# Performance work log

Hardware: AMD Instinct MI355X
Metric: run time of the kernel (lower is better)

## Reference

```python
import jax, jax.numpy as jnp
import numpy as np

NEG_SLOPE = 0.2  # LeakyReLU slope in GAT attention
HEADS = 10

def gat_layer(x, src, dst, W, a_src, a_dst, b, H, C, N):
    # x: [N, F_in]; W: [F_in, H*C]; a_src/a_dst: [H, C]; b: [C]
    h = (x @ W).reshape(N, H, C)                      # [N, H, C]
    e_s = (h * a_src).sum(-1)                         # [N, H]
    e_d = (h * a_dst).sum(-1)                         # [N, H]
    e = jax.nn.leaky_relu(e_s[src] + e_d[dst], NEG_SLOPE)  # [E, H]
    m = jax.ops.segment_max(e, dst, num_segments=N)
    m = jnp.where(jnp.isfinite(m), m, 0.0)
    p = jnp.exp(e - m[dst])                           # [E, H]
    denom = jax.ops.segment_sum(p, dst, num_segments=N)
    alpha = p / (denom[dst] + 1e-16)                  # [E, H]
    out = jax.ops.segment_sum(alpha[:, :, None] * h[src], dst, num_segments=N)  # [N, H, C]
    return out.mean(1) + b                            # heads averaged (concat=False)


def setup_inputs() -> dict:
    key = jax.random.key(0)
    N, E, F, CLS = 10000, 160000, 24, 24
    ks = jax.random.split(key, 24)
    p = lambda k, shp: 0.1 * jax.random.normal(k, shp, dtype=jnp.float32)
    return {
        "x": jax.random.normal(ks[0], (N, F), dtype=jnp.float32),
        "edge_index": jax.random.randint(ks[1], (2, E), 0, N, dtype=jnp.int64),
        "batch": jnp.sort(jax.random.randint(ks[2], (N,), 0, 64, dtype=jnp.int64)),
        "W0": p(ks[3], (F, 16)), "b0": p(ks[4], (16,)),
        "Wc1": p(ks[5], (16, HEADS * 32)), "as1": p(ks[6], (HEADS, 32)), "ad1": p(ks[7], (HEADS, 32)), "bc1": p(ks[8], (32,)),
        "Wc2": p(ks[9], (32, HEADS * 64)), "as2": p(ks[10], (HEADS, 64)), "ad2": p(ks[11], (HEADS, 64)), "bc2": p(ks[12], (64,)),
        "Wc3": p(ks[13], (64, HEADS * 128)), "as3": p(ks[14], (HEADS, 128)), "ad3": p(ks[15], (HEADS, 128)), "bc3": p(ks[16], (128,)),
        "W1": p(ks[17], (128, 256)), "b1": p(ks[18], (256,)),
        "W2": p(ks[19], (256, CLS)), "b2": p(ks[20], (CLS,)),
    }


def reference(x, edge_index, batch, W0, b0, Wc1, as1, ad1, bc1, Wc2, as2, ad2, bc2,
              Wc3, as3, ad3, bc3, W1, b1, W2, b2):
    N = x.shape[0]
    self_loop = jnp.arange(N, dtype=edge_index.dtype)
    src = jnp.concatenate([edge_index[0], self_loop])
    dst = jnp.concatenate([edge_index[1], self_loop])
    h = jax.nn.elu(x @ W0 + b0)
    h = jax.nn.elu(gat_layer(h, src, dst, Wc1, as1, ad1, bc1, HEADS, 32, N))
    h = jax.nn.elu(gat_layer(h, src, dst, Wc2, as2, ad2, bc2, HEADS, 64, N))
    h = jax.nn.elu(gat_layer(h, src, dst, Wc3, as3, ad3, bc3, HEADS, 128, N))
    h = jax.nn.elu(h @ W1 + b1)
    # dropout is identity in eval mode
    logits = h @ W2 + b2
    return jax.nn.log_softmax(logits, axis=1)
```

## Files before the change

kernel.cpp:

```cpp
#include <hip/hip_runtime.h>
#include <hip/hip_bf16.h>
#include <math.h>

#define NHEADS 10

typedef unsigned short ushort_t;
typedef unsigned int uint_t;

typedef __attribute__((ext_vector_type(4))) float f32x4;
typedef __attribute__((ext_vector_type(8))) short short8;

__device__ __forceinline__ float bu2f(ushort_t u){ return __uint_as_float(((uint_t)u)<<16); }
__device__ __forceinline__ ushort_t f2bu(float f){
    uint_t b = __float_as_uint(f);
    return (ushort_t)((b + 0x7FFFu + ((b>>16)&1u)) >> 16);
}

__global__ void k_count(const int* eidx, int E, int N, int* cnt){
    int e = blockIdx.x*blockDim.x + threadIdx.x;
    int ET = E + N;
    if(e >= ET) return;
    int d = (e < E) ? eidx[E + e] : (e - E);
    atomicAdd(&cnt[d], 1);
}

__global__ void k_scan(int* cnt, int N, int ET, int* indptr){
    __shared__ int lds[1024];
    int t = threadIdx.x;
    int chunk = (N + 1023)/1024;
    int base = t*chunk;
    int s = 0;
    for(int i=0;i<chunk;i++){ int idx=base+i; if(idx<N) s += cnt[idx]; }
    lds[t]=s;
    __syncthreads();
    for(int off=1; off<1024; off<<=1){
        int v = (t>=off)? lds[t-off] : 0;
        __syncthreads();
        lds[t]+=v;
        __syncthreads();
    }
    int run = lds[t]-s;
    for(int i=0;i<chunk;i++){
        int idx=base+i;
        if(idx<N){
            int c = cnt[idx];
            indptr[idx]=run;
            cnt[idx]=run;
            run += c;
        }
    }
    if(t==0) indptr[N]=ET;
}

__global__ void k_fill(const int* eidx, int E, int N, int* cursor, int* srcs){
    int e = blockIdx.x*blockDim.x + threadIdx.x;
    int ET = E + N;
    if(e >= ET) return;
    int s, d;
    if(e < E){ s = eidx[e]; d = eidx[E+e]; } else { s = e-E; d = e-E; }
    int pos = atomicAdd(&cursor[d], 1);
    srcs[pos] = s;
}

__global__ void k_sortw(const int* indptr, int* srcs, int N){
    int wid  = (blockIdx.x*blockDim.x + threadIdx.x) >> 6;
    int lane = threadIdx.x & 63;
    if(wid >= N) return;
    int p0 = indptr[wid], p1 = indptr[wid+1];
    int deg = p1 - p0;
    if(deg <= 1) return;
    if(deg <= 64){
        int v = (lane < deg) ? srcs[p0+lane] : 0x7FFFFFFF;
        #pragma unroll
        for(int k=2; k<=64; k<<=1){
            #pragma unroll
            for(int j=k>>1; j>0; j>>=1){
                int partner = __shfl_xor(v, j, 64);
                bool dir   = ((lane & k) == 0);
                bool small = ((lane & j) == 0);
                int mn = min(v, partner), mx = max(v, partner);
                v = (dir == small) ? mn : mx;
            }
        }
        if(lane < deg) srcs[p0+lane] = v;
    } else if(lane == 0){
        for(int i=p0+1;i<p1;i++){
            int v2 = srcs[i]; int j=i-1;
            while(j>=p0 && srcs[j]>v2){ srcs[j+1]=srcs[j]; j--; }
            srcs[j+1]=v2;
        }
    }
}

__global__ void k_trans(const float* __restrict__ W, ushort_t* __restrict__ WT,
                        int K, int KP, int HC){
    int idx = blockIdx.x*blockDim.x + threadIdx.x;
    if(idx >= HC*KP) return;
    int c = idx / KP, k = idx % KP;
    WT[idx] = (k < K) ? f2bu(W[(size_t)k*HC + c]) : (ushort_t)0;
}

__global__ void k_fc0(const float* x, const float* W0, const float* b0, float* out, int N){
    int idx = blockIdx.x*blockDim.x+threadIdx.x;
    if(idx >= N*16) return;
    int n = idx>>4, c = idx&15;
    float acc = b0[c];
    #pragma unroll
    for(int k=0;k<24;k++) acc += x[n*24+k] * W0[k*16+c];
    out[idx] = acc>0.f ? acc : expm1f(acc);
}

template<int K, int KP, int EPI, int OUTBF16>
__global__ void __launch_bounds__(256, 4)
k_gemm(const float* __restrict__ A, const ushort_t* __restrict__ BT,
       const float* __restrict__ bias, void* __restrict__ Cmat,
       int N, int HC){
    int t = threadIdx.x;
    int w = t >> 6, lane = t & 63;
    int lr = lane & 15, lk = lane >> 4;
    int row0 = blockIdx.x*64, col0 = blockIdx.y*64;
    int row = row0 + w*16 + lr;

    f32x4 acc[4];
    #pragma unroll
    for(int f=0; f<4; f++) acc[f] = (f32x4){0.f,0.f,0.f,0.f};

    #pragma unroll
    for(int kb = 0; kb < K; kb += 32){
        int k0 = kb + lk*8;
        short8 af = {0,0,0,0,0,0,0,0};
        if(row < N && k0 < K){
            const float* ap = &A[(size_t)row*K + k0];
            float4 a0 = *(const float4*)ap;
            float4 a1 = *(const float4*)(ap + 4);
            af[0]=(short)f2bu(a0.x); af[1]=(short)f2bu(a0.y);
            af[2]=(short)f2bu(a0.z); af[3]=(short)f2bu(a0.w);
            af[4]=(short)f2bu(a1.x); af[5]=(short)f2bu(a1.y);
            af[6]=(short)f2bu(a1.z); af[7]=(short)f2bu(a1.w);
        }
        #pragma unroll
        for(int f=0; f<4; f++){
            int col = col0 + f*16 + lr;
            short8 bf = *(const short8*)&BT[(size_t)col*KP + k0];
            acc[f] = __builtin_amdgcn_mfma_f32_16x16x32_bf16(af, bf, acc[f], 0, 0, 0);
        }
    }

    #pragma unroll
    for(int f=0; f<4; f++){
        #pragma unroll
        for(int j=0; j<4; j++){
            int r = row0 + w*16 + lk*4 + j;
            if(r >= N) continue;
            int col = col0 + f*16 + lr;
            float v = acc[f][j];
            if(EPI){
                v += bias[col];
                v = v>0.f ? v : expm1f(v);
            }
            if(OUTBF16) ((ushort_t*)Cmat)[(size_t)r*HC + col] = f2bu(v);
            else        ((float*)Cmat)[(size_t)r*HC + col] = v;
        }
    }
}

template<int C>
__global__ void k_attn(const ushort_t* hf, const float* a_s, const float* a_d,
                       float* es, float* ed, int N){
    int tid = blockIdx.x*blockDim.x + threadIdx.x;
    if(tid >= N*NHEADS*4) return;
    int q   = tid & 3;
    int idx = tid >> 2;
    int n = idx/NHEADS, h = idx%NHEADS;
    constexpr int CQ = C/4;
    const ushort_t* hp = hf + (size_t)n*NHEADS*C + h*C + q*CQ;
    const float* asp = a_s + h*C + q*CQ;
    const float* adp = a_d + h*C + q*CQ;
    float s=0.f, d=0.f;
    #pragma unroll
    for(int cb=0; cb<CQ/8; cb++){
        uint4 qv = *(const uint4*)(hp + cb*8);
        uint_t uu[4] = {qv.x, qv.y, qv.z, qv.w};
        #pragma unroll
        for(int j=0;j<4;j++){
            float f0 = __uint_as_float(uu[j]<<16);
            float f1 = __uint_as_float(uu[j] & 0xFFFF0000u);
            int c = cb*8 + j*2;
            s += f0*asp[c] + f1*asp[c+1];
            d += f0*adp[c] + f1*adp[c+1];
        }
    }
    s += __shfl_xor(s, 1, 64); s += __shfl_xor(s, 2, 64);
    d += __shfl_xor(d, 1, 64); d += __shfl_xor(d, 2, 64);
    if(q == 0){ es[idx]=s; ed[idx]=d; }
}

template<int C>
__global__ void __launch_bounds__(256, 4)
k_fused(const int* __restrict__ indptr, const int* __restrict__ srcs,
        const float* __restrict__ es, const float* __restrict__ ed,
        const ushort_t* __restrict__ hf, const float* __restrict__ bc,
        float* __restrict__ out, int N)
{
    __shared__ float wlds[4][64*NHEADS];
    __shared__ float stat[4][NHEADS];
    __shared__ int   degs[4];
    int wslot = threadIdx.x >> 6;
    int lane  = threadIdx.x & 63;
    int n = (blockIdx.x << 2) + wslot;
    bool valid = (n < N);
    int p0 = 0, deg = 0;
    if(valid){ p0 = indptr[n]; deg = indptr[n+1] - p0; }
    if(lane == 0) degs[wslot] = deg;
    __syncthreads();
    int maxdeg = max(max(degs[0],degs[1]), max(degs[2],degs[3]));
    int nch = (maxdeg + 63) >> 6;
    float* wl = wlds[wslot];

    int e6 = lane/10, h6 = lane%10;
    float edv = (valid && lane < 60) ? ed[n*NHEADS + h6] : 0.f;

    float den = 0.f;
    for(int c = 0; c < nch; c++){
        int base = c << 6;
        int lim = deg - base; if(lim > 64) lim = 64;
        if(valid && lane < 60){
            for(int i = e6; i < lim; i += 6){
                float v = es[(size_t)srcs[p0+base+i]*NHEADS + h6] + edv;
                v = (v >= 0.f) ? v : 0.2f*v;
                wl[i*NHEADS + h6] = expf(fminf(v, 60.f));
            }
        }
        __syncthreads();
        if(valid && lane < NHEADS){
            for(int i = 0; i < lim; i++) den += wl[i*NHEADS + lane];
        }
        if(nch > 1) __syncthreads();
    }
    if(valid && lane < NHEADS) stat[wslot][lane] = 1.f/(den + 1e-30f);
    __syncthreads();

    constexpr int TPN = C/8;
    constexpr int EG  = 64/TPN;
    int local = lane % TPN, eg = lane / TPN;
    int c8 = local*8;
    float dinv_r[NHEADS];
    #pragma unroll
    for(int h=0; h<NHEADS; h++) dinv_r[h] = stat[wslot][h];
    float acc[8];
    #pragma unroll
    for(int i=0;i<8;i++) acc[i]=0.f;

    for(int c = 0; c < nch; c++){
        int base = c << 6;
        int lim = deg - base; if(lim > 64) lim = 64;
        if(nch > 1){
            if(valid && lane < 60){
                for(int i = e6; i < lim; i += 6){
                    float v = es[(size_t)srcs[p0+base+i]*NHEADS + h6] + edv;
                    v = (v >= 0.f) ? v : 0.2f*v;
                    wl[i*NHEADS + h6] = expf(fminf(v, 60.f));
                }
            }
            __syncthreads();
        }
        if(valid){
            for(int i = eg; i < lim; i += EG){
                int s = srcs[p0+base+i];
                const ushort_t* hp = hf + (size_t)s*NHEADS*C + c8;
                const float* wp = &wl[i*NHEADS];
                #pragma unroll
                for(int h=0;h<NHEADS;h++){
                    uint4 q = *(const uint4*)(hp + h*C);
                    float wd = wp[h]*dinv_r[h];
                    acc[0] += wd * __uint_as_float(q.x<<16);
                    acc[1] += wd * __uint_as_float(q.x & 0xFFFF0000u);
                    acc[2] += wd * __uint_as_float(q.y<<16);
                    acc[3] += wd * __uint_as_float(q.y & 0xFFFF0000u);
                    acc[4] += wd * __uint_as_float(q.z<<16);
                    acc[5] += wd * __uint_as_float(q.z & 0xFFFF0000u);
                    acc[6] += wd * __uint_as_float(q.w<<16);
                    acc[7] += wd * __uint_as_float(q.w & 0xFFFF0000u);
                }
            }
        }
        if(nch > 1) __syncthreads();
    }

    #pragma unroll
    for(int s = TPN; s < 64; s <<= 1){
        #pragma unroll
        for(int i=0;i<8;i++) acc[i] += __shfl_xor(acc[i], s, 64);
    }
    if(valid && eg == 0){
        float4 v0, v1;
        #pragma unroll
        for(int i=0;i<8;i++){
            float v = acc[i]*(1.f/NHEADS) + bc[c8+i];
            v = v>0.f ? v : expm1f(v);
            if(i<4) ((float*)&v0)[i] = v; else ((float*)&v1)[i-4] = v;
        }
        *(float4*)&out[(size_t)n*C + c8]     = v0;
        *(float4*)&out[(size_t)n*C + c8 + 4] = v1;
    }
}

__global__ void k_head(const float* hin, const float* W2, const float* b2v, float* out, int N){
    int grp  = threadIdx.x/32;
    int lane = threadIdx.x%32;
    int n = blockIdx.x*8 + grp;
    if(n>=N) return;
    float acc = -1e30f;
    if(lane < 24){
        acc = b2v[lane];
        for(int k=0;k<256;k++) acc += hin[n*256+k]*W2[k*24+lane];
    }
    float mx = acc;
    for(int off=16; off; off>>=1) mx = fmaxf(mx, __shfl_xor(mx, off, 32));
    float ex = (lane<24)? expf(acc-mx) : 0.f;
    float sm = ex;
    for(int off=16; off; off>>=1) sm += __shfl_xor(sm, off, 32);
    if(lane<24) out[n*24+lane] = acc - mx - logf(sm);
}

extern "C" void kernel_launch(void* const* d_in, const int* in_sizes, int n_in,
                              void* d_out, int out_size, void* d_ws, size_t ws_size,
                              hipStream_t stream) {
    const float* x   = (const float*)d_in[0];
    const int*  eidx = (const int*)d_in[1];
    const float* W0 = (const float*)d_in[3];  const float* b0 = (const float*)d_in[4];
    const float* Wc1= (const float*)d_in[5];  const float* as1= (const float*)d_in[6];
    const float* ad1= (const float*)d_in[7];  const float* bc1= (const float*)d_in[8];
    const float* Wc2= (const float*)d_in[9];  const float* as2= (const float*)d_in[10];
    const float* ad2= (const float*)d_in[11]; const float* bc2= (const float*)d_in[12];
    const float* Wc3= (const float*)d_in[13]; const float* as3= (const float*)d_in[14];
    const float* ad3= (const float*)d_in[15]; const float* bc3= (const float*)d_in[16];
    const float* W1 = (const float*)d_in[17]; const float* b1 = (const float*)d_in[18];
    const float* W2 = (const float*)d_in[19]; const float* b2 = (const float*)d_in[20];
    float* out = (float*)d_out;

    const int N  = in_sizes[0]/24;
    const int E  = in_sizes[1]/2;
    const int ET = E + N;

    char* w = (char*)d_ws;
    size_t off = 0;
    auto alloc = [&](size_t bytes)->void* {
        void* p = w + off;
        off = (off + bytes + 255) & ~(size_t)255;
        return p;
    };
    int*   cnt    = (int*)  alloc((size_t)N*4);
    int*   indptr = (int*)  alloc((size_t)(N+1)*4);
    int*   srcs   = (int*)  alloc((size_t)ET*4);
    float* es     = (float*)alloc((size_t)N*NHEADS*4);
    float* ed     = (float*)alloc((size_t)N*NHEADS*4);
    float* nfA    = (float*)alloc((size_t)N*256*4);
    float* nfB    = (float*)alloc((size_t)N*256*4);
    ushort_t* hf  = (ushort_t*)alloc((size_t)N*1280*2);
    ushort_t* WT1 = (ushort_t*)alloc((size_t)320*32*2);
    ushort_t* WT2 = (ushort_t*)alloc((size_t)640*32*2);
    ushort_t* WT3 = (ushort_t*)alloc((size_t)1280*64*2);
    ushort_t* WT4 = (ushort_t*)alloc((size_t)256*128*2);

    k_trans<<<(320*32+255)/256,256,0,stream>>>(Wc1, WT1, 16, 32, 320);
    k_trans<<<(640*32+255)/256,256,0,stream>>>(Wc2, WT2, 32, 32, 640);
    k_trans<<<(1280*64+255)/256,256,0,stream>>>(Wc3, WT3, 64, 64, 1280);
    k_trans<<<(256*128+255)/256,256,0,stream>>>(W1, WT4, 128, 128, 256);

    hipMemsetAsync(cnt, 0, (size_t)N*4, stream);
    int gE = (ET+255)/256;
    k_count<<<gE,256,0,stream>>>(eidx, E, N, cnt);
    k_scan <<<1,1024,0,stream>>>(cnt, N, ET, indptr);
    k_fill <<<gE,256,0,stream>>>(eidx, E, N, cnt, srcs);
    k_sortw<<<((size_t)N*64+255)/256,256,0,stream>>>(indptr, srcs, N);

    int gA   = (N*NHEADS*4+255)/256;
    int gRow = (N+63)/64;
    int gNode = (N+3)/4;

    k_fc0<<<(N*16+255)/256,256,0,stream>>>(x, W0, b0, nfA, N);

    k_gemm<16,32,0,1><<<dim3(gRow,320/64),256,0,stream>>>(nfA, WT1, nullptr, hf, N, 320);
    k_attn<32><<<gA,256,0,stream>>>(hf, as1, ad1, es, ed, N);
    k_fused<32><<<gNode,256,0,stream>>>(indptr, srcs, es, ed, hf, bc1, nfB, N);

    k_gemm<32,32,0,1><<<dim3(gRow,640/64),256,0,stream>>>(nfB, WT2, nullptr, hf, N, 640);
    k_attn<64><<<gA,256,0,stream>>>(hf, as2, ad2, es, ed, N);
    k_fused<64><<<gNode,256,0,stream>>>(indptr, srcs, es, ed, hf, bc2, nfA, N);

    k_gemm<64,64,0,1><<<dim3(gRow,1280/64),256,0,stream>>>(nfA, WT3, nullptr, hf, N, 1280);
    k_attn<128><<<gA,256,0,stream>>>(hf, as3, ad3, es, ed, N);
    k_fused<128><<<gNode,256,0,stream>>>(indptr, srcs, es, ed, hf, bc3, nfB, N);

    k_gemm<128,128,1,0><<<dim3(gRow,256/64),256,0,stream>>>(nfB, WT4, b1, nfA, N, 256);
    k_head<<<(N+7)/8,256,0,stream>>>(nfA, W2, b2, out, N);
}
```

Baseline: 298.2 us.

## Phase neighbor gathers by source-index window and merge weight transpose launches

Splits the sorted source neighbors of each node into P index windows and walks them phase by phase, with a block barrier between phases. The waves of a block then gather feature rows from the same region of the bf16 feature array at roughly the same time, which should improve L2 locality. The four weight-transpose launches are also merged into one kernel to save launch overhead. The cost is up to P extra __syncthreads per block, and the multi-chunk path now folds the inverse denominator into the stored weights for chunks after the first.

```diff
diff --git a/kernel.cpp b/kernel.cpp
--- a/kernel.cpp
+++ b/kernel.cpp
@@ -92,12 +92,17 @@
     }
 }
 
-__global__ void k_trans(const float* __restrict__ W, ushort_t* __restrict__ WT,
-                        int K, int KP, int HC){
+__global__ void k_trans_all(const float* __restrict__ W1c,const float* __restrict__ W2c,
+                            const float* __restrict__ W3c,const float* __restrict__ W4c,
+                            ushort_t* T1,ushort_t* T2,ushort_t* T3,ushort_t* T4){
     int idx = blockIdx.x*blockDim.x + threadIdx.x;
-    if(idx >= HC*KP) return;
-    int c = idx / KP, k = idx % KP;
-    WT[idx] = (k < K) ? f2bu(W[(size_t)k*HC + c]) : (ushort_t)0;
+    if(idx < 10240){ int c=idx/32, k=idx%32; T1[idx] = (k<16)? f2bu(W1c[(size_t)k*320+c]) : (ushort_t)0; return; }
+    idx -= 10240;
+    if(idx < 20480){ int c=idx/32, k=idx%32; T2[idx] = f2bu(W2c[(size_t)k*640+c]); return; }
+    idx -= 20480;
+    if(idx < 81920){ int c=idx/64, k=idx%64; T3[idx] = f2bu(W3c[(size_t)k*1280+c]); return; }
+    idx -= 81920;
+    if(idx < 32768){ int c=idx/128, k=idx%128; T4[idx] = f2bu(W4c[(size_t)k*256+c]); return; }
 }
 
 __global__ void k_fc0(const float* x, const float* W0, const float* b0, float* out, int N){
@@ -195,7 +200,7 @@
     if(q == 0){ es[idx]=s; ed[idx]=d; }
 }
 
-template<int C>
+template<int C, int P>
 __global__ void __launch_bounds__(256, 4)
 k_fused(const int* __restrict__ indptr, const int* __restrict__ srcs,
         const float* __restrict__ es, const float* __restrict__ ed,
@@ -251,22 +256,14 @@
     #pragma unroll
     for(int i=0;i<8;i++) acc[i]=0.f;
 
-    for(int c = 0; c < nch; c++){
-        int base = c << 6;
-        int lim = deg - base; if(lim > 64) lim = 64;
-        if(nch > 1){
-            if(valid && lane < 60){
-                for(int i = e6; i < lim; i += 6){
-                    float v = es[(size_t)srcs[p0+base+i]*NHEADS + h6] + edv;
-                    v = (v >= 0.f) ? v : 0.2f*v;
-                    wl[i*NHEADS + h6] = expf(fminf(v, 60.f));
-                }
-            }
-            __syncthreads();
-        }
-        if(valid){
-            for(int i = eg; i < lim; i += EG){
-                int s = srcs[p0+base+i];
+    if(nch == 1){
+        int lim = deg;
+        int win = (N + P - 1)/P;
+        int i = eg;
+        for(int ph = 0; ph < P; ph++){
+            int bound = win*(ph+1);
+            while(i < lim && srcs[p0+i] < bound){
+                int s = srcs[p0+i];
                 const ushort_t* hp = hf + (size_t)s*NHEADS*C + c8;
                 const float* wp = &wl[i*NHEADS];
                 #pragma unroll
@@ -282,9 +279,48 @@
                     acc[6] += wd * __uint_as_float(q.w<<16);
                     acc[7] += wd * __uint_as_float(q.w & 0xFFFF0000u);
                 }
-            }
-        }
-        if(nch > 1) __syncthreads();
+                i += EG;
+            }
+            __syncthreads();
+        }
+    } else {
+        for(int c = 0; c < nch; c++){
+            int base = c << 6;
+            int lim = deg - base; if(lim > 64) lim = 64;
+            if(c > 0){
+                if(valid && lane < 60){
+                    for(int i = e6; i < lim; i += 6){
+                        float v = es[(size_t)srcs[p0+base+i]*NHEADS + h6] + edv;
+                        v = (v >= 0.f) ? v : 0.2f*v;
+                        wl[i*NHEADS + h6] = expf(fminf(v, 60.f)) * dinv_r[h6];
+                    }
+                }
+                __syncthreads();
+            }
+            if(valid){
+                for(int i = eg; i < lim; i += EG){
+                    int s = srcs[p0+base+i];
+                    const ushort_t* hp = hf + (size_t)s*NHEADS*C + c8;
+                    const float* wp = &wl[i*NHEADS];
+                    float fac = (c == 0) ? 1.f : (1.f/1.f);
+                    #pragma unroll
+                    for(int h=0;h<NHEADS;h++){
+                        uint4 q = *(const uint4*)(hp + h*C);
+                        float wd = (c == 0) ? wp[h]*dinv_r[h] : wp[h];
+                        acc[0] += wd * __uint_as_float(q.x<<16);
+                        acc[1] += wd * __uint_as_float(q.x & 0xFFFF0000u);
+                        acc[2] += wd * __uint_as_float(q.y<<16);
+                        acc[3] += wd * __uint_as_float(q.y & 0xFFFF0000u);
+                        acc[4] += wd * __uint_as_float(q.z<<16);
+                        acc[5] += wd * __uint_as_float(q.z & 0xFFFF0000u);
+                        acc[6] += wd * __uint_as_float(q.w<<16);
+                        acc[7] += wd * __uint_as_float(q.w & 0xFFFF0000u);
+                    }
+                    (void)fac;
+                }
+            }
+            __syncthreads();
+        }
     }
 
     #pragma unroll
@@ -363,10 +399,7 @@
     ushort_t* WT3 = (ushort_t*)alloc((size_t)1280*64*2);
     ushort_t* WT4 = (ushort_t*)alloc((size_t)256*128*2);
 
-    k_trans<<<(320*32+255)/256,256,0,stream>>>(Wc1, WT1, 16, 32, 320);
-    k_trans<<<(640*32+255)/256,256,0,stream>>>(Wc2, WT2, 32, 32, 640);
-    k_trans<<<(1280*64+255)/256,256,0,stream>>>(Wc3, WT3, 64, 64, 1280);
-    k_trans<<<(256*128+255)/256,256,0,stream>>>(W1, WT4, 128, 128, 256);
+    k_trans_all<<<(145408+255)/256,256,0,stream>>>(Wc1, Wc2, Wc3, W1, WT1, WT2, WT3, WT4);
 
     hipMemsetAsync(cnt, 0, (size_t)N*4, stream);
     int gE = (ET+255)/256;
@@ -383,15 +416,15 @@
 
     k_gemm<16,32,0,1><<<dim3(gRow,320/64),256,0,stream>>>(nfA, WT1, nullptr, hf, N, 320);
     k_attn<32><<<gA,256,0,stream>>>(hf, as1, ad1, es, ed, N);
-    k_fused<32><<<gNode,256,0,stream>>>(indptr, srcs, es, ed, hf, bc1, nfB, N);
+    k_fused<32,2><<<gNode,256,0,stream>>>(indptr, srcs, es, ed, hf, bc1, nfB, N);
 
     k_gemm<32,32,0,1><<<dim3(gRow,640/64),256,0,stream>>>(nfB, WT2, nullptr, hf, N, 640);
     k_attn<64><<<gA,256,0,stream>>>(hf, as2, ad2, es, ed, N);
-    k_fused<64><<<gNode,256,0,stream>>>(indptr, srcs, es, ed, hf, bc2, nfA, N);
+    k_fused<64,4><<<gNode,256,0,stream>>>(indptr, srcs, es, ed, hf, bc2, nfA, N);
 
     k_gemm<64,64,0,1><<<dim3(gRow,1280/64),256,0,stream>>>(nfA, WT3, nullptr, hf, N, 1280);
     k_attn<128><<<gA,256,0,stream>>>(hf, as3, ad3, es, ed, N);
-    k_fused<128><<<gNode,256,0,stream>>>(indptr, srcs, es, ed, hf, bc3, nfB, N);
+    k_fused<128,8><<<gNode,256,0,stream>>>(indptr, srcs, es, ed, hf, bc3, nfB, N);
 
     k_gemm<128,128,1,0><<<dim3(gRow,256/64),256,0,stream>>>(nfB, WT4, b1, nfA, N, 256);
     k_head<<<(N+7)/8,256,0,stream>>>(nfA, W2, b2, out, N);
```

New measurement: 293.6 us. No clear change (-1.5%).

## Split GAT aggregation into weight, source-windowed gather, and reduce kernels

Applied to the files above, without the earlier changes.

The fused per-node softmax+aggregation kernel is split into three kernels. The first computes normalized edge weights into a global buffer. The second gathers neighbor features in eight source-index windows, one window per block, using per-node range offsets computed during the sort, so concurrent blocks touch a narrower slice of the feature table and hit cache more often. The third sums the bf16 partials and applies bias and ELU. The four weight-transpose launches are also merged into one. This costs extra global traffic for the weight and partial buffers, three times as many launches per layer, and bf16 rounding of the partial sums.

```diff
diff --git a/kernel.cpp b/kernel.cpp
--- a/kernel.cpp
+++ b/kernel.cpp
@@ -62,42 +62,60 @@
     srcs[pos] = s;
 }
 
-__global__ void k_sortw(const int* indptr, int* srcs, int N){
+__global__ void k_sortw(const int* indptr, int* srcs, int* rng, int N){
     int wid  = (blockIdx.x*blockDim.x + threadIdx.x) >> 6;
     int lane = threadIdx.x & 63;
     if(wid >= N) return;
     int p0 = indptr[wid], p1 = indptr[wid+1];
     int deg = p1 - p0;
-    if(deg <= 1) return;
+    int win = (N + 7) >> 3;
     if(deg <= 64){
-        int v = (lane < deg) ? srcs[p0+lane] : 0x7FFFFFFF;
-        #pragma unroll
-        for(int k=2; k<=64; k<<=1){
+        int v = (lane < deg && deg > 1) ? srcs[p0+lane] : 0x7FFFFFFF;
+        if(deg == 1 && lane == 0) v = srcs[p0];
+        if(deg > 1){
             #pragma unroll
-            for(int j=k>>1; j>0; j>>=1){
-                int partner = __shfl_xor(v, j, 64);
-                bool dir   = ((lane & k) == 0);
-                bool small = ((lane & j) == 0);
-                int mn = min(v, partner), mx = max(v, partner);
-                v = (dir == small) ? mn : mx;
+            for(int k=2; k<=64; k<<=1){
+                #pragma unroll
+                for(int j=k>>1; j>0; j>>=1){
+                    int partner = __shfl_xor(v, j, 64);
+                    bool dir   = ((lane & k) == 0);
+                    bool small = ((lane & j) == 0);
+                    int mn = min(v, partner), mx = max(v, partner);
+                    v = (dir == small) ? mn : mx;
+                }
             }
-        }
-        if(lane < deg) srcs[p0+lane] = v;
+            if(lane < deg) srcs[p0+lane] = v;
+        }
+        #pragma unroll
+        for(int r=0; r<8; r++){
+            unsigned long long m = __ballot(v < r*win);
+            if(lane == 0) rng[wid*8 + r] = p0 + (int)__popcll(m);
+        }
     } else if(lane == 0){
         for(int i=p0+1;i<p1;i++){
             int v2 = srcs[i]; int j=i-1;
             while(j>=p0 && srcs[j]>v2){ srcs[j+1]=srcs[j]; j--; }
             srcs[j+1]=v2;
         }
-    }
-}
-
-__global__ void k_trans(const float* __restrict__ W, ushort_t* __restrict__ WT,
-                        int K, int KP, int HC){
+        for(int r=0;r<8;r++){
+            int b=r*win, c=0;
+            for(int i=p0;i<p1;i++) if(srcs[i]<b) c++;
+            rng[wid*8+r]=p0+c;
+        }
+    }
+}
+
+__global__ void k_trans_all(const float* __restrict__ W1c,const float* __restrict__ W2c,
+                            const float* __restrict__ W3c,const float* __restrict__ W4c,
+                            ushort_t* T1,ushort_t* T2,ushort_t* T3,ushort_t* T4){
     int idx = blockIdx.x*blockDim.x + threadIdx.x;
-    if(idx >= HC*KP) return;
-    int c = idx / KP, k = idx % KP;
-    WT[idx] = (k < K) ? f2bu(W[(size_t)k*HC + c]) : (ushort_t)0;
+    if(idx < 10240){ int c=idx/32, k=idx%32; T1[idx] = (k<16)? f2bu(W1c[(size_t)k*320+c]) : (ushort_t)0; return; }
+    idx -= 10240;
+    if(idx < 20480){ int c=idx/32, k=idx%32; T2[idx] = f2bu(W2c[(size_t)k*640+c]); return; }
+    idx -= 20480;
+    if(idx < 81920){ int c=idx/64, k=idx%64; T3[idx] = f2bu(W3c[(size_t)k*1280+c]); return; }
+    idx -= 81920;
+    if(idx < 32768){ int c=idx/128, k=idx%128; T4[idx] = f2bu(W4c[(size_t)k*256+c]); return; }
 }
 
 __global__ void k_fc0(const float* x, const float* W0, const float* b0, float* out, int N){
@@ -195,14 +213,12 @@
     if(q == 0){ es[idx]=s; ed[idx]=d; }
 }
 
-template<int C>
 __global__ void __launch_bounds__(256, 4)
-k_fused(const int* __restrict__ indptr, const int* __restrict__ srcs,
-        const float* __restrict__ es, const float* __restrict__ ed,
-        const ushort_t* __restrict__ hf, const float* __restrict__ bc,
-        float* __restrict__ out, int N)
+k_wts(const int* __restrict__ indptr, const int* __restrict__ srcs,
+      const float* __restrict__ es, const float* __restrict__ ed,
+      float* __restrict__ wbuf, int N)
 {
-    __shared__ float wlds[4][64*NHEADS];
+    __shared__ float wl4[4][64*NHEADS];
     __shared__ float stat[4][NHEADS];
     __shared__ int   degs[4];
     int wslot = threadIdx.x >> 6;
@@ -215,7 +231,7 @@
     __syncthreads();
     int maxdeg = max(max(degs[0],degs[1]), max(degs[2],degs[3]));
     int nch = (maxdeg + 63) >> 6;
-    float* wl = wlds[wslot];
+    float* wl = wl4[wslot];
 
     int e6 = lane/10, h6 = lane%10;
     float edv = (valid && lane < 60) ? ed[n*NHEADS + h6] : 0.f;
@@ -228,81 +244,110 @@
             for(int i = e6; i < lim; i += 6){
                 float v = es[(size_t)srcs[p0+base+i]*NHEADS + h6] + edv;
                 v = (v >= 0.f) ? v : 0.2f*v;
-                wl[i*NHEADS + h6] = expf(fminf(v, 60.f));
+                float wv = expf(fminf(v, 60.f));
+                wl[i*NHEADS + h6] = wv;
+                wbuf[(size_t)(p0+base+i)*NHEADS + h6] = wv;
             }
         }
         __syncthreads();
         if(valid && lane < NHEADS){
             for(int i = 0; i < lim; i++) den += wl[i*NHEADS + lane];
         }
-        if(nch > 1) __syncthreads();
+        __syncthreads();
     }
     if(valid && lane < NHEADS) stat[wslot][lane] = 1.f/(den + 1e-30f);
     __syncthreads();
-
+    if(valid && lane < 60){
+        float dv = stat[wslot][h6];
+        for(int i = e6; i < deg; i += 6)
+            wbuf[(size_t)(p0+i)*NHEADS + h6] *= dv;
+    }
+}
+
+template<int C>
+__global__ void __launch_bounds__(256, 4)
+k_gath(const int* __restrict__ indptr, const int* __restrict__ srcs,
+       const int* __restrict__ rng, const float* __restrict__ wbuf,
+       const ushort_t* __restrict__ hf, ushort_t* __restrict__ part, int N)
+{
     constexpr int TPN = C/8;
     constexpr int EG  = 64/TPN;
+    int wslot = threadIdx.x >> 6;
+    int lane  = threadIdx.x & 63;
+    int r = blockIdx.x & 7;
+    int n = (blockIdx.x >> 3)*4 + wslot;
+    if(n >= N) return;
+    int lo = rng[n*8 + r];
+    int hi = (r < 7) ? rng[n*8 + r + 1] : indptr[n+1];
     int local = lane % TPN, eg = lane / TPN;
     int c8 = local*8;
-    float dinv_r[NHEADS];
-    #pragma unroll
-    for(int h=0; h<NHEADS; h++) dinv_r[h] = stat[wslot][h];
     float acc[8];
     #pragma unroll
     for(int i=0;i<8;i++) acc[i]=0.f;
-
-    for(int c = 0; c < nch; c++){
-        int base = c << 6;
-        int lim = deg - base; if(lim > 64) lim = 64;
-        if(nch > 1){
-            if(valid && lane < 60){
-                for(int i = e6; i < lim; i += 6){
-                    float v = es[(size_t)srcs[p0+base+i]*NHEADS + h6] + edv;
-                    v = (v >= 0.f) ? v : 0.2f*v;
-                    wl[i*NHEADS + h6] = expf(fminf(v, 60.f));
-                }
-            }
-            __syncthreads();
-        }
-        if(valid){
-            for(int i = eg; i < lim; i += EG){
-                int s = srcs[p0+base+i];
-                const ushort_t* hp = hf + (size_t)s*NHEADS*C + c8;
-                const float* wp = &wl[i*NHEADS];
-                #pragma unroll
-                for(int h=0;h<NHEADS;h++){
-                    uint4 q = *(const uint4*)(hp + h*C);
-                    float wd = wp[h]*dinv_r[h];
-                    acc[0] += wd * __uint_as_float(q.x<<16);
-                    acc[1] += wd * __uint_as_float(q.x & 0xFFFF0000u);
-                    acc[2] += wd * __uint_as_float(q.y<<16);
-                    acc[3] += wd * __uint_as_float(q.y & 0xFFFF0000u);
-                    acc[4] += wd * __uint_as_float(q.z<<16);
-                    acc[5] += wd * __uint_as_float(q.z & 0xFFFF0000u);
-                    acc[6] += wd * __uint_as_float(q.w<<16);
-                    acc[7] += wd * __uint_as_float(q.w & 0xFFFF0000u);
-                }
-            }
-        }
-        if(nch > 1) __syncthreads();
-    }
-
+    for(int p = lo + eg; p < hi; p += EG){
+        int s = srcs[p];
+        const ushort_t* hp = hf + (size_t)s*NHEADS*C + c8;
+        const float* wp = wbuf + (size_t)p*NHEADS;
+        #pragma unroll
+        for(int h=0;h<NHEADS;h++){
+            uint4 q = *(const uint4*)(hp + h*C);
+            float wd = wp[h];
+            acc[0] += wd * __uint_as_float(q.x<<16);
+            acc[1] += wd * __uint_as_float(q.x & 0xFFFF0000u);
+            acc[2] += wd * __uint_as_float(q.y<<16);
+            acc[3] += wd * __uint_as_float(q.y & 0xFFFF0000u);
+            acc[4] += wd * __uint_as_float(q.z<<16);
+            acc[5] += wd * __uint_as_float(q.z & 0xFFFF0000u);
+            acc[6] += wd * __uint_as_float(q.w<<16);
+            acc[7] += wd * __uint_as_float(q.w & 0xFFFF0000u);
+        }
+    }
     #pragma unroll
     for(int s = TPN; s < 64; s <<= 1){
         #pragma unroll
         for(int i=0;i<8;i++) acc[i] += __shfl_xor(acc[i], s, 64);
     }
-    if(valid && eg == 0){
-        float4 v0, v1;
-        #pragma unroll
-        for(int i=0;i<8;i++){
-            float v = acc[i]*(1.f/NHEADS) + bc[c8+i];
-            v = v>0.f ? v : expm1f(v);
-            if(i<4) ((float*)&v0)[i] = v; else ((float*)&v1)[i-4] = v;
-        }
-        *(float4*)&out[(size_t)n*C + c8]     = v0;
-        *(float4*)&out[(size_t)n*C + c8 + 4] = v1;
-    }
+    if(eg == 0){
+        uint4 u;
+        u.x = (uint_t)f2bu(acc[0]) | ((uint_t)f2bu(acc[1])<<16);
+        u.y = (uint_t)f2bu(acc[2]) | ((uint_t)f2bu(acc[3])<<16);
+        u.z = (uint_t)f2bu(acc[4]) | ((uint_t)f2bu(acc[5])<<16);
+        u.w = (uint_t)f2bu(acc[6]) | ((uint_t)f2bu(acc[7])<<16);
+        *(uint4*)&part[((size_t)r*N + n)*C + c8] = u;
+    }
+}
+
+template<int C>
+__global__ void k_red(const ushort_t* __restrict__ part, const float* __restrict__ bc,
+                      float* __restrict__ out, int N){
+    int tid = blockIdx.x*blockDim.x + threadIdx.x;
+    if(tid >= N*(C/8)) return;
+    int n = tid/(C/8);
+    int c8 = (tid%(C/8))*8;
+    float s[8];
+    #pragma unroll
+    for(int i=0;i<8;i++) s[i]=0.f;
+    #pragma unroll
+    for(int r=0;r<8;r++){
+        uint4 u = *(const uint4*)&part[((size_t)r*N + n)*C + c8];
+        s[0] += __uint_as_float(u.x<<16);
+        s[1] += __uint_as_float(u.x & 0xFFFF0000u);
+        s[2] += __uint_as_float(u.y<<16);
+        s[3] += __uint_as_float(u.y & 0xFFFF0000u);
+        s[4] += __uint_as_float(u.z<<16);
+        s[5] += __uint_as_float(u.z & 0xFFFF0000u);
+        s[6] += __uint_as_float(u.w<<16);
+        s[7] += __uint_as_float(u.w & 0xFFFF0000u);
+    }
+    float4 v0, v1;
+    #pragma unroll
+    for(int i=0;i<8;i++){
+        float v = s[i]*(1.f/NHEADS) + bc[c8+i];
+        v = v>0.f ? v : expm1f(v);
+        if(i<4) ((float*)&v0)[i] = v; else ((float*)&v1)[i-4] = v;
+    }
+    *(float4*)&out[(size_t)n*C + c8]     = v0;
+    *(float4*)&out[(size_t)n*C + c8 + 4] = v1;
 }
 
 __global__ void k_head(const float* hin, const float* W2, const float* b2v, float* out, int N){
@@ -353,45 +398,52 @@
     int*   cnt    = (int*)  alloc((size_t)N*4);
     int*   indptr = (int*)  alloc((size_t)(N+1)*4);
     int*   srcs   = (int*)  alloc((size_t)ET*4);
+    int*   rng    = (int*)  alloc((size_t)N*8*4);
     float* es     = (float*)alloc((size_t)N*NHEADS*4);
     float* ed     = (float*)alloc((size_t)N*NHEADS*4);
+    float* wbuf   = (float*)alloc((size_t)ET*NHEADS*4);
     float* nfA    = (float*)alloc((size_t)N*256*4);
     float* nfB    = (float*)alloc((size_t)N*256*4);
     ushort_t* hf  = (ushort_t*)alloc((size_t)N*1280*2);
+    ushort_t* part= (ushort_t*)alloc((size_t)8*N*128*2);
     ushort_t* WT1 = (ushort_t*)alloc((size_t)320*32*2);
     ushort_t* WT2 = (ushort_t*)alloc((size_t)640*32*2);
     ushort_t* WT3 = (ushort_t*)alloc((size_t)1280*64*2);
     ushort_t* WT4 = (ushort_t*)alloc((size_t)256*128*2);
 
-    k_trans<<<(320*32+255)/256,256,0,stream>>>(Wc1, WT1, 16, 32, 320);
-    k_trans<<<(640*32+255)/256,256,0,stream>>>(Wc2, WT2, 32, 32, 640);
-    k_trans<<<(1280*64+255)/256,256,0,stream>>>(Wc3, WT3, 64, 64, 1280);
-    k_trans<<<(256*128+255)/256,256,0,stream>>>(W1, WT4, 128, 128, 256);
+    k_trans_all<<<(145408+255)/256,256,0,stream>>>(Wc1, Wc2, Wc3, W1, WT1, WT2, WT3, WT4);
 
     hipMemsetAsync(cnt, 0, (size_t)N*4, stream);
     int gE = (ET+255)/256;
     k_count<<<gE,256,0,stream>>>(eidx, E, N, cnt);
     k_scan <<<1,1024,0,stream>>>(cnt, N, ET, indptr);
     k_fill <<<gE,256,0,stream>>>(eidx, E, N, cnt, srcs);
-    k_sortw<<<((size_t)N*64+255)/256,256,0,stream>>>(indptr, srcs, N);
-
-    int gA   = (N*NHEADS*4+255)/256;
-    int gRow = (N+63)/64;
+    k_sortw<<<((size_t)N*64+255)/256,256,0,stream>>>(indptr, srcs, rng, N);
+
+    int gA    = (N*NHEADS*4+255)/256;
+    int gRow  = (N+63)/64;
     int gNode = (N+3)/4;
+    int gGath = ((N+3)/4)*8;
 
     k_fc0<<<(N*16+255)/256,256,0,stream>>>(x, W0, b0, nfA, N);
 
     k_gemm<16,32,0,1><<<dim3(gRow,320/64),256,0,stream>>>(nfA, WT1, nullptr, hf, N, 320);
     k_attn<32><<<gA,256,0,stream>>>(hf, as1, ad1, es, ed, N);
-    k_fused<32><<<gNode,256,0,stream>>>(indptr, srcs, es, ed, hf, bc1, nfB, N);
+    k_wts<<<gNode,256,0,stream>>>(indptr, srcs, es, ed, wbuf, N);
+    k_gath<32><<<gGath,256,0,stream>>>(indptr, srcs, rng, wbuf, hf, part, N);
+    k_red<32><<<(N*4+255)/256,256,0,stream>>>(part, bc1, nfB, N);
 
     k_gemm<32,32,0,1><<<dim3(gRow,640/64),256,0,stream>>>(nfB, WT2, nullptr, hf, N, 640);
     k_attn<64><<<gA,256,0,stream>>>(hf, as2, ad2, es, ed, N);
-    k_fused<64><<<gNode,256,0,stream>>>(indptr, srcs, es, ed, hf, bc2, nfA, N);
+    k_wts<<<gNode,256,0,stream>>>(indptr, srcs, es, ed, wbuf, N);
+    k_gath<64><<<gGath,256,0,stream>>>(indptr, srcs, rng, wbuf, hf, part, N);
+    k_red<64><<<(N*8+255)/256,256,0,stream>>>(part, bc2, nfA, N);
 
     k_gemm<64,64,0,1><<<dim3(gRow,1280/64),256,0,stream>>>(nfA, WT3, nullptr, hf, N, 1280);
     k_attn<128><<<gA,256,0,stream>>>(hf, as3, ad3, es, ed, N);
-    k_fused<128><<<gNode,256,0,stream>>>(indptr, srcs, es, ed, hf, bc3, nfB, N);
+    k_wts<<<gNode,256,0,stream>>>(indptr, srcs, es, ed, wbuf, N);
+    k_gath<128><<<gGath,256,0,stream>>>(indptr, srcs, rng, wbuf, hf, part, N);
+    k_red<128><<<(N*16+255)/256,256,0,stream>>>(part, bc3, nfB, N);
 
     k_gemm<128,128,1,0><<<dim3(gRow,256/64),256,0,stream>>>(nfB, WT4, b1, nfA, N, 256);
     k_head<<<(N+7)/8,256,0,stream>>>(nfA, W2, b2, out, N);
```

Result: slower. 367.4 us (+23.2%).
